# Optimization experiments

Hardware: AMD Instinct MI355X
Metric: run time of the kernel (lower is better)

The kernel has to match this reference:

```python
import jax, jax.numpy as jnp
import numpy as np

CUTOFF = 3  # cutoff_freq default in low_pass_filter


def _low_pass(x):
    # full 2D FFT over (H, W), keep only the 4 corner blocks of size CUTOFF
    H, W = x.shape[-2], x.shape[-1]
    f = jnp.fft.fftn(x, axes=(-2, -1))
    mask = jnp.zeros((H, W), dtype=x.dtype)
    c = CUTOFF
    mask = mask.at[:c, :c].set(1).at[:c, -c:].set(1).at[-c:, :c].set(1).at[-c:, -c:].set(1)
    return jnp.abs(jnp.fft.ifftn(f * mask, axes=(-2, -1)))


def setup_inputs() -> dict:
    key = jax.random.key(0)
    k_x, k_w1, k_b1, k_w2, k_b2 = jax.random.split(key, 5)
    n_feat = 8
    B, C, H, W = 32, 3, 512, 512
    x = jax.random.uniform(k_x, (B, C, H, W), dtype=jnp.float32)
    # 1x1 convs == channel-mixing matrices; kaiming-ish scale
    w1 = jax.random.normal(k_w1, (n_feat, C), dtype=jnp.float32) * (1.0 / np.sqrt(C))
    b1 = jax.random.normal(k_b1, (n_feat,), dtype=jnp.float32) * 0.01
    w2 = jax.random.normal(k_w2, (C, n_feat), dtype=jnp.float32) * (1.0 / np.sqrt(n_feat))
    b2 = jax.random.normal(k_b2, (C,), dtype=jnp.float32) * 0.01
    return {"x": x, "w1": w1, "b1": b1, "w2": w2, "b2": b2}


def reference(x, w1, b1, w2, b2):
    lp = _low_pass(x)                                        # [B,3,H,W]
    h = jax.nn.relu(jnp.einsum('bchw,fc->bfhw', lp, w1) + b1[None, :, None, None])
    y = jnp.einsum('bfhw,cf->bchw', h, w2) + b2[None, :, None, None]
    return jnp.clip(y + lp, 0.0, 1.0)
```

## Files before the change

### kernel.cpp

```cpp
#include <hip/hip_runtime.h>
#include <math.h>


#define WS_TS 0
#define WS_PP 8192
#define WS_A  65536
constexpr int NPART = 8;

#define CJ1 0.99992470183914450299f
#define CJ2 0.99969881869620422012f
#define CJ3 0.99932238458834954375f
#define CJ4 0.99879545620517239271f
#define SJ1 0.01227153828571992539f
#define SJ2 0.02454122852291228803f
#define SJ3 0.03680722294135883171f
#define SJ4 0.04906767432741801425f

__global__ __launch_bounds__(256, 4) void k_colsum(const float* __restrict__ x,
                                                   float* __restrict__ ws) {
    __shared__ float buf[3][64][57];
    float* A = ws + WS_A;
    int img = blockIdx.x >> 3;
    int hgrp = blockIdx.x & 7;
    int t = threadIdx.x;
    int v = t >> 6;
    int lane = t & 63;
    int R0 = hgrp * 64 + v * 16;
    const float* xb = x + (size_t)img * 262144 + (size_t)R0 * 512 + lane * 4;

    const float TH = 6.28318530717958647692f / 512.0f;
    float bc, bs;
    sincosf(TH * (float)R0, &bs, &bc);

    float aA[7][4], aB[7][4];
#pragma unroll
    for (int c = 0; c < 7; ++c)
#pragma unroll
        for (int q = 0; q < 4; ++q) { aA[c][q] = 0.f; aB[c][q] = 0.f; }

    const float CJr[4] = {1.f, CJ1, CJ2, CJ3};
    const float SJr[4] = {0.f, SJ1, SJ2, SJ3};

#pragma unroll
    for (int b = 0; b < 4; ++b) {
        float4 L[8];
#pragma unroll
        for (int rr = 0; rr < 4; ++rr) {
            L[rr * 2 + 0] = *(const float4*)(xb + (size_t)(b * 4 + rr) * 512);
            L[rr * 2 + 1] = *(const float4*)(xb + (size_t)(b * 4 + rr) * 512 + 256);
        }
#pragma unroll
        for (int rr = 0; rr < 4; ++rr) {
            float c1 = bc * CJr[rr] - bs * SJr[rr];
            float s1 = bs * CJr[rr] + bc * SJr[rr];
            float c2 = c1 * c1 - s1 * s1;
            float s2 = 2.f * c1 * s1;
            float c3 = c1 * c2 - s1 * s2;
            float s3 = s1 * c2 + c1 * s2;
            float xa[4] = {L[rr * 2].x, L[rr * 2].y, L[rr * 2].z, L[rr * 2].w};
            float xbv[4] = {L[rr * 2 + 1].x, L[rr * 2 + 1].y, L[rr * 2 + 1].z, L[rr * 2 + 1].w};
#pragma unroll
            for (int q = 0; q < 4; ++q) {
                aA[0][q] += xa[q];
                aA[1][q] = fmaf(xa[q], c1, aA[1][q]);  aA[2][q] = fmaf(-xa[q], s1, aA[2][q]);
                aA[3][q] = fmaf(xa[q], c2, aA[3][q]);  aA[4][q] = fmaf(-xa[q], s2, aA[4][q]);
                aA[5][q] = fmaf(xa[q], c3, aA[5][q]);  aA[6][q] = fmaf(-xa[q], s3, aA[6][q]);
                aB[0][q] += xbv[q];
                aB[1][q] = fmaf(xbv[q], c1, aB[1][q]); aB[2][q] = fmaf(-xbv[q], s1, aB[2][q]);
                aB[3][q] = fmaf(xbv[q], c2, aB[3][q]); aB[4][q] = fmaf(-xbv[q], s2, aB[4][q]);
                aB[5][q] = fmaf(xbv[q], c3, aB[5][q]); aB[6][q] = fmaf(-xbv[q], s3, aB[6][q]);
            }
        }
        if (b < 3) {
            float nb = bc * CJ4 - bs * SJ4;
            bs = bs * CJ4 + bc * SJ4;
            bc = nb;
        }
    }

    if (v != 0) {
        float* r = &buf[v - 1][lane][0];
#pragma unroll
        for (int c = 0; c < 7; ++c)
#pragma unroll
            for (int q = 0; q < 4; ++q) {
                r[c * 4 + q] = aA[c][q];
                r[28 + c * 4 + q] = aB[c][q];
            }
    }
    __syncthreads();
    if (v == 0) {
#pragma unroll
        for (int u = 0; u < 3; ++u) {
            const float* r = &buf[u][lane][0];
#pragma unroll
            for (int c = 0; c < 7; ++c)
#pragma unroll
                for (int q = 0; q < 4; ++q) {
                    aA[c][q] += r[c * 4 + q];
                    aB[c][q] += r[28 + c * 4 + q];
                }
        }
        float* Ab = A + (((size_t)img * NPART + hgrp) * 8) * 512 + lane * 4;
        const int pl[7] = {0, 2, 3, 4, 5, 6, 7};
#pragma unroll
        for (int c = 0; c < 7; ++c) {
            *(float4*)(Ab + (size_t)pl[c] * 512)       = make_float4(aA[c][0], aA[c][1], aA[c][2], aA[c][3]);
            *(float4*)(Ab + (size_t)pl[c] * 512 + 256) = make_float4(aB[c][0], aB[c][1], aB[c][2], aB[c][3]);
        }
        *(float4*)(Ab + 1 * 512)       = make_float4(0.f, 0.f, 0.f, 0.f);
        *(float4*)(Ab + 1 * 512 + 256) = make_float4(0.f, 0.f, 0.f, 0.f);
    }
}

__global__ __launch_bounds__(256) void k_proj(float* __restrict__ ws) {
    int t = threadIdx.x;
    const float TH = 6.28318530717958647692f / 512.0f;
    if (blockIdx.x == 768) {
        const int mv[6] = {0, 1, 2, -3, -2, -1};
        for (int h = t; h < 512; h += 256) {
            float* tsp = ws + WS_TS + h * 12;
#pragma unroll
            for (int i = 0; i < 6; ++i) {
                int r = ((mv[i] * h) % 512 + 512) & 511;
                float s, c;
                sincosf(TH * (float)r, &s, &c);
                tsp[2 * i] = c; tsp[2 * i + 1] = s;
            }
        }
        return;
    }
    __shared__ float As[8][64];
    const float* A = ws + WS_A;
    float* Pp = ws + WS_PP;
    int img = blockIdx.x >> 3;
    int seg = blockIdx.x & 7;

    {
        int plane = t >> 5;
        int wl = (t & 31) * 2;
        float2 L[8];
#pragma unroll
        for (int hg = 0; hg < NPART; ++hg)
            L[hg] = *(const float2*)(A + (((size_t)img * NPART + hg) * 8 + plane) * 512 + seg * 64 + wl);
        float ax = 0.f, ay = 0.f;
#pragma unroll
        for (int hg = 0; hg < NPART; ++hg) { ax += L[hg].x; ay += L[hg].y; }
        As[plane][wl] = ax;
        As[plane][wl + 1] = ay;
    }
    __syncthreads();

    if (t < 28) {
        int k = t / 7, mi = t % 7;
        float m = (float)(mi - 3);
        float cm, sm, pc, ps;
        sincosf(-m * TH, &sm, &cm);
        sincosf(-m * TH * (float)(seg * 64), &ps, &pc);
        const float* Ar_ = &As[2 * k][0];
        const float* Ai_ = &As[2 * k + 1][0];
        float pre = 0.f, pim = 0.f;
#pragma unroll 4
        for (int j = 0; j < 64; ++j) {
            float Ar = Ar_[j], Ai = Ai_[j];
            pre += Ar * pc - Ai * ps;
            pim += Ar * ps + Ai * pc;
            float n = pc * cm - ps * sm;
            ps = ps * cm + pc * sm;
            pc = n;
        }
        float* o = Pp + ((size_t)img * 8 + seg) * 56;
        o[t * 2] = pre;
        o[t * 2 + 1] = pim;
    }
}

__global__ __launch_bounds__(256) void k_out(const float* __restrict__ ws,
                                             const float* __restrict__ w1,
                                             const float* __restrict__ b1,
                                             const float* __restrict__ w2,
                                             const float* __restrict__ b2,
                                             float* __restrict__ out) {
    const float* tabS = ws + WS_TS;
    const float* Pp = ws + WS_PP;
    __shared__ float F_lds[3][56];
    __shared__ float T[4][3][12];
    int t = threadIdx.x;
    int blk = blockIdx.x;
    int b = blk >> 7;
    int h0 = (blk & 127) << 2;

    if (t < 168) {
        int c = t / 56, comp = t % 56;
        const float* pp = Pp + ((size_t)(b * 3 + c) * 8) * 56 + comp;
        float s = 0.f;
#pragma unroll
        for (int g = 0; g < 8; ++g) s += pp[g * 56];
        F_lds[c][comp] = s;
    }

    float rw1[8][3], rb1[8], rw2[3][8], rb2[3];
#pragma unroll
    for (int f_ = 0; f_ < 8; ++f_) {
        rb1[f_] = b1[f_];
#pragma unroll
        for (int c = 0; c < 3; ++c) rw1[f_][c] = w1[f_ * 3 + c];
    }
#pragma unroll
    for (int c = 0; c < 3; ++c) {
        rb2[c] = b2[c];
#pragma unroll
        for (int f_ = 0; f_ < 8; ++f_) rw2[c][f_] = w2[c * 8 + f_];
    }
    __syncthreads();

    if (t < 72) {
        int rl = t / 18, rem = t % 18;
        int c = rem / 6, kc = rem % 6;
        int h = h0 + rl;
        const float* th = tabS + h * 12;
        int m_kc = (kc < 3) ? kc : kc - 6;
        const float inv = 1.0f / (512.0f * 512.0f);
        float tre = 0.f, tim = 0.f;
#pragma unroll
        for (int kr = 0; kr < 6; ++kr) {
            int kk, mi; float csign;
            if (kr < 3) { kk = kr;     mi = m_kc + 3; csign =  1.f; }
            else        { kk = 6 - kr; mi = 3 - m_kc; csign = -1.f; }
            int pair = kk * 7 + mi;
            float fr = F_lds[c][pair * 2] * inv;
            float fi = F_lds[c][pair * 2 + 1] * csign * inv;
            float cc = th[kr * 2], ss = th[kr * 2 + 1];
            tre += fr * cc - fi * ss;
            tim += fr * ss + fi * cc;
        }
        T[rl][c][kc * 2]     = tre;
        T[rl][c][kc * 2 + 1] = tim;
    }
    __syncthreads();

    int rl = t >> 6, lane = t & 63;
    int h = h0 + rl;
    float A0r[3], A0i[3], U1r[3], U1i[3], V1r[3], V1i[3];
    float U2r[3], U2i[3], V2r[3], V2i[3], Br[3], Bi[3];
#pragma unroll
    for (int c = 0; c < 3; ++c) {
        const float* Tc = T[rl][c];
        A0r[c] = Tc[0];  A0i[c] = Tc[1];
        float t1r = Tc[2],  t1i = Tc[3];
        float t2r = Tc[4],  t2i = Tc[5];
        float bmr = Tc[6],  bmi = Tc[7];
        float m2r = Tc[8],  m2i = Tc[9];
        float m1r = Tc[10], m1i = Tc[11];
        U1r[c] = t1r + m1r; U1i[c] = t1i + m1i;
        V1r[c] = t1r - m1r; V1i[c] = t1i - m1i;
        U2r[c] = t2r + m2r; U2i[c] = t2i + m2i;
        V2r[c] = t2r - m2r; V2i[c] = t2i - m2i;
        Br[c] = bmr; Bi[c] = bmi;
    }
    const float* tw = tabS + lane * 12;
    float c1 = tw[2], s1 = tw[3];
    float c2 = tw[4], s2 = tw[5];
    float c3 = tw[6], s3 = -tw[7];
    const float K = 0.70710678118654752440f;
    float* ob = out + ((size_t)(b * 3) * 512 + h) * 512;

#pragma unroll
    for (int j = 0; j < 8; ++j) {
        int w = lane + 64 * j;
        float lp[3];
#pragma unroll
        for (int c = 0; c < 3; ++c) {
            float re = A0r[c] + U1r[c] * c1 - V1i[c] * s1
                              + U2r[c] * c2 - V2i[c] * s2
                              + Br[c] * c3 + Bi[c] * s3;
            float im = A0i[c] + U1i[c] * c1 + V1r[c] * s1
                              + U2i[c] * c2 + V2r[c] * s2
                              + Bi[c] * c3 - Br[c] * s3;
            lp[c] = sqrtf(re * re + im * im);
        }
        float hid[8];
#pragma unroll
        for (int f_ = 0; f_ < 8; ++f_) {
            float v = rb1[f_] + lp[0] * rw1[f_][0] + lp[1] * rw1[f_][1] + lp[2] * rw1[f_][2];
            hid[f_] = fmaxf(v, 0.0f);
        }
#pragma unroll
        for (int c = 0; c < 3; ++c) {
            float y = rb2[c] + lp[c];
#pragma unroll
            for (int f_ = 0; f_ < 8; ++f_) y += hid[f_] * rw2[c][f_];
            y = fminf(fmaxf(y, 0.0f), 1.0f);
            ob[(size_t)c * 262144 + w] = y;
        }
        if (j < 7) {
            float nc1 = K * (c1 - s1), ns1 = K * (c1 + s1);
            float nc2 = -s2,           ns2 = c2;
            float nc3 = -K * (c3 + s3), ns3 = K * (c3 - s3);
            c1 = nc1; s1 = ns1; c2 = nc2; s2 = ns2; c3 = nc3; s3 = ns3;
        }
    }
}

extern "C" void kernel_launch(void* const* d_in, const int* in_sizes, int n_in,
                              void* d_out, int out_size, void* d_ws, size_t ws_size,
                              hipStream_t stream) {
    const float* x  = (const float*)d_in[0];
    const float* w1 = (const float*)d_in[1];
    const float* b1 = (const float*)d_in[2];
    const float* w2 = (const float*)d_in[3];
    const float* b2 = (const float*)d_in[4];
    float* out = (float*)d_out;
    float* ws = (float*)d_ws;

    hipLaunchKernelGGL(k_colsum, dim3(96 * 8), dim3(256), 0, stream, x, ws);
    hipLaunchKernelGGL(k_proj, dim3(769), dim3(256), 0, stream, ws);
    hipLaunchKernelGGL(k_out, dim3(4096), dim3(256), 0, stream, ws, w1, b1, w2, b2, out);
}
```

Baseline: 64.54 us.

## Stream column-sum rows through triple-buffered LDS with async global-to-LDS loads

The column-sum kernel now copies 4-row chunks of the image straight into a three-slot LDS ring using global_load_lds, keeping two chunks in flight while the current one is reduced. Each thread owns one column pair for the whole 64-row group, which removes the cross-wave shared-memory reduction and the 56-register accumulator arrays. This adds a barrier per chunk and relies on hand-written vmcnt waits, and each thread now does only a few FMAs per LDS read.

```diff
diff --git a/kernel.cpp b/kernel.cpp
--- a/kernel.cpp
+++ b/kernel.cpp
@@ -16,101 +16,90 @@
 #define SJ3 0.03680722294135883171f
 #define SJ4 0.04906767432741801425f
 
-__global__ __launch_bounds__(256, 4) void k_colsum(const float* __restrict__ x,
-                                                   float* __restrict__ ws) {
-    __shared__ float buf[3][64][57];
+__global__ __launch_bounds__(256) void k_colsum(const float* __restrict__ x,
+                                                float* __restrict__ ws) {
+    __shared__ float tile[3 * 2048];
     float* A = ws + WS_A;
     int img = blockIdx.x >> 3;
     int hgrp = blockIdx.x & 7;
     int t = threadIdx.x;
-    int v = t >> 6;
+    int wave = t >> 6;
     int lane = t & 63;
-    int R0 = hgrp * 64 + v * 16;
-    const float* xb = x + (size_t)img * 262144 + (size_t)R0 * 512 + lane * 4;
+    const float* xb = x + (size_t)img * 262144 + (size_t)(hgrp * 64) * 512;
+
+    auto stage = [&](int b, int tt) {
+#pragma unroll
+        for (int j = 0; j < 2; ++j) {
+            int c = wave * 2 + j;
+            const float* g = xb + (size_t)tt * 2048 + c * 256 + lane * 4;
+            float* l = &tile[b * 2048 + c * 256];
+            __builtin_amdgcn_global_load_lds(
+                (const __attribute__((address_space(1))) void*)g,
+                (__attribute__((address_space(3))) void*)l, 16, 0, 0);
+        }
+    };
 
     const float TH = 6.28318530717958647692f / 512.0f;
     float bc, bs;
-    sincosf(TH * (float)R0, &bs, &bc);
-
-    float aA[7][4], aB[7][4];
-#pragma unroll
-    for (int c = 0; c < 7; ++c)
-#pragma unroll
-        for (int q = 0; q < 4; ++q) { aA[c][q] = 0.f; aB[c][q] = 0.f; }
-
+    sincosf(TH * (float)(hgrp * 64), &bs, &bc);
     const float CJr[4] = {1.f, CJ1, CJ2, CJ3};
     const float SJr[4] = {0.f, SJ1, SJ2, SJ3};
 
-#pragma unroll
-    for (int b = 0; b < 4; ++b) {
-        float4 L[8];
-#pragma unroll
-        for (int rr = 0; rr < 4; ++rr) {
-            L[rr * 2 + 0] = *(const float4*)(xb + (size_t)(b * 4 + rr) * 512);
-            L[rr * 2 + 1] = *(const float4*)(xb + (size_t)(b * 4 + rr) * 512 + 256);
-        }
-#pragma unroll
-        for (int rr = 0; rr < 4; ++rr) {
-            float c1 = bc * CJr[rr] - bs * SJr[rr];
-            float s1 = bs * CJr[rr] + bc * SJr[rr];
+    float aA[7], aB[7];
+#pragma unroll
+    for (int c = 0; c < 7; ++c) { aA[c] = 0.f; aB[c] = 0.f; }
+
+    stage(0, 0);
+    stage(1, 1);
+    asm volatile("s_waitcnt vmcnt(2)" ::: "memory");
+    __syncthreads();
+
+    int bcur = 0;
+    for (int tt = 0; tt < 16; ++tt) {
+        int bnext = bcur + 2; if (bnext >= 3) bnext -= 3;
+        if (tt + 2 < 16) stage(bnext, tt + 2);
+
+        const float* tb = &tile[bcur * 2048];
+#pragma unroll
+        for (int j = 0; j < 4; ++j) {
+            float c1 = bc * CJr[j] - bs * SJr[j];
+            float s1 = bs * CJr[j] + bc * SJr[j];
             float c2 = c1 * c1 - s1 * s1;
             float s2 = 2.f * c1 * s1;
             float c3 = c1 * c2 - s1 * s2;
             float s3 = s1 * c2 + c1 * s2;
-            float xa[4] = {L[rr * 2].x, L[rr * 2].y, L[rr * 2].z, L[rr * 2].w};
-            float xbv[4] = {L[rr * 2 + 1].x, L[rr * 2 + 1].y, L[rr * 2 + 1].z, L[rr * 2 + 1].w};
-#pragma unroll
-            for (int q = 0; q < 4; ++q) {
-                aA[0][q] += xa[q];
-                aA[1][q] = fmaf(xa[q], c1, aA[1][q]);  aA[2][q] = fmaf(-xa[q], s1, aA[2][q]);
-                aA[3][q] = fmaf(xa[q], c2, aA[3][q]);  aA[4][q] = fmaf(-xa[q], s2, aA[4][q]);
-                aA[5][q] = fmaf(xa[q], c3, aA[5][q]);  aA[6][q] = fmaf(-xa[q], s3, aA[6][q]);
-                aB[0][q] += xbv[q];
-                aB[1][q] = fmaf(xbv[q], c1, aB[1][q]); aB[2][q] = fmaf(-xbv[q], s1, aB[2][q]);
-                aB[3][q] = fmaf(xbv[q], c2, aB[3][q]); aB[4][q] = fmaf(-xbv[q], s2, aB[4][q]);
-                aB[5][q] = fmaf(xbv[q], c3, aB[5][q]); aB[6][q] = fmaf(-xbv[q], s3, aB[6][q]);
-            }
-        }
-        if (b < 3) {
+            float xa = tb[j * 512 + t];
+            float xc = tb[j * 512 + t + 256];
+            aA[0] += xa;
+            aA[1] = fmaf(xa, c1, aA[1]);  aA[2] = fmaf(-xa, s1, aA[2]);
+            aA[3] = fmaf(xa, c2, aA[3]);  aA[4] = fmaf(-xa, s2, aA[4]);
+            aA[5] = fmaf(xa, c3, aA[5]);  aA[6] = fmaf(-xa, s3, aA[6]);
+            aB[0] += xc;
+            aB[1] = fmaf(xc, c1, aB[1]);  aB[2] = fmaf(-xc, s1, aB[2]);
+            aB[3] = fmaf(xc, c2, aB[3]);  aB[4] = fmaf(-xc, s2, aB[4]);
+            aB[5] = fmaf(xc, c3, aB[5]);  aB[6] = fmaf(-xc, s3, aB[6]);
+        }
+        {
             float nb = bc * CJ4 - bs * SJ4;
             bs = bs * CJ4 + bc * SJ4;
             bc = nb;
         }
-    }
-
-    if (v != 0) {
-        float* r = &buf[v - 1][lane][0];
-#pragma unroll
-        for (int c = 0; c < 7; ++c)
-#pragma unroll
-            for (int q = 0; q < 4; ++q) {
-                r[c * 4 + q] = aA[c][q];
-                r[28 + c * 4 + q] = aB[c][q];
-            }
-    }
-    __syncthreads();
-    if (v == 0) {
-#pragma unroll
-        for (int u = 0; u < 3; ++u) {
-            const float* r = &buf[u][lane][0];
-#pragma unroll
-            for (int c = 0; c < 7; ++c)
-#pragma unroll
-                for (int q = 0; q < 4; ++q) {
-                    aA[c][q] += r[c * 4 + q];
-                    aB[c][q] += r[28 + c * 4 + q];
-                }
-        }
-        float* Ab = A + (((size_t)img * NPART + hgrp) * 8) * 512 + lane * 4;
-        const int pl[7] = {0, 2, 3, 4, 5, 6, 7};
-#pragma unroll
-        for (int c = 0; c < 7; ++c) {
-            *(float4*)(Ab + (size_t)pl[c] * 512)       = make_float4(aA[c][0], aA[c][1], aA[c][2], aA[c][3]);
-            *(float4*)(Ab + (size_t)pl[c] * 512 + 256) = make_float4(aB[c][0], aB[c][1], aB[c][2], aB[c][3]);
-        }
-        *(float4*)(Ab + 1 * 512)       = make_float4(0.f, 0.f, 0.f, 0.f);
-        *(float4*)(Ab + 1 * 512 + 256) = make_float4(0.f, 0.f, 0.f, 0.f);
-    }
+
+        if (tt + 2 < 16) asm volatile("s_waitcnt vmcnt(2)" ::: "memory");
+        else             asm volatile("s_waitcnt vmcnt(0)" ::: "memory");
+        __syncthreads();
+        bcur = bcur + 1; if (bcur >= 3) bcur -= 3;
+    }
+
+    float* Ab = A + (((size_t)img * NPART + hgrp) * 8) * 512;
+    const int pl[7] = {0, 2, 3, 4, 5, 6, 7};
+#pragma unroll
+    for (int c = 0; c < 7; ++c) {
+        Ab[(size_t)pl[c] * 512 + t]       = aA[c];
+        Ab[(size_t)pl[c] * 512 + t + 256] = aB[c];
+    }
+    Ab[(size_t)1 * 512 + t]       = 0.f;
+    Ab[(size_t)1 * 512 + t + 256] = 0.f;
 }
 
 __global__ __launch_bounds__(256) void k_proj(float* __restrict__ ws) {
@@ -313,7 +302,7 @@
     float* out = (float*)d_out;
     float* ws = (float*)d_ws;
 
-    hipLaunchKernelGGL(k_colsum, dim3(96 * 8), dim3(256), 0, stream, x, ws);
+    hipLaunchKernelGGL(k_colsum, dim3(96 * NPART), dim3(256), 0, stream, x, ws);
     hipLaunchKernelGGL(k_proj, dim3(769), dim3(256), 0, stream, ws);
     hipLaunchKernelGGL(k_out, dim3(4096), dim3(256), 0, stream, ws, w1, b1, w2, b2, out);
 }
```

Result: no change. 64.03 us (-0.8%).
